# Kernel tuning notes

Hardware: AMD Instinct MI355X
Metric: run time of the kernel (lower is better)

Reference implementation:

```python
import jax, jax.numpy as jnp
import numpy as np

N_NODES = 100000
N_EDGES = 1200000
D_IN = 16
D_EDGE = 4
H = 64


def setup_inputs() -> dict:
    key = jax.random.key(0)
    ks = jax.random.split(key, 20)
    s = 0.05
    inp = {
        "src": jax.random.randint(ks[0], (N_EDGES,), 0, N_NODES),
        "dst": jax.random.randint(ks[1], (N_EDGES,), 0, N_NODES),
        "t": jax.random.uniform(ks[2], (N_EDGES,), dtype=jnp.float32),
        "x": jax.random.normal(ks[3], (N_NODES, D_IN), dtype=jnp.float32),
        "edge_attr": jax.random.normal(ks[4], (N_EDGES, D_EDGE), dtype=jnp.float32),
        # x_encoder
        "Wx": jax.random.normal(ks[5], (D_IN, H), dtype=jnp.float32) * s,
        "bx": jnp.zeros((H,), dtype=jnp.float32),
        # TransformerConv (heads=1, concat=False)
        "Wq": jax.random.normal(ks[6], (H, H), dtype=jnp.float32) * s,
        "bq": jnp.zeros((H,), dtype=jnp.float32),
        "Wk": jax.random.normal(ks[7], (H, H), dtype=jnp.float32) * s,
        "bk": jnp.zeros((H,), dtype=jnp.float32),
        "Wv": jax.random.normal(ks[8], (H, H), dtype=jnp.float32) * s,
        "bv": jnp.zeros((H,), dtype=jnp.float32),
        "We": jax.random.normal(ks[9], (D_EDGE, H), dtype=jnp.float32) * s,  # lin_edge, bias=False
        "Ws": jax.random.normal(ks[10], (H, H), dtype=jnp.float32) * s,  # lin_skip (root weight)
        "bs": jnp.zeros((H,), dtype=jnp.float32),
        # MLP head
        "W1": jax.random.normal(ks[11], (H, 8), dtype=jnp.float32) * s,
        "b1": jnp.zeros((8,), dtype=jnp.float32),
        "W2": jax.random.normal(ks[12], (8, 1), dtype=jnp.float32) * s,
        "b2": jnp.zeros((1,), dtype=jnp.float32),
    }
    return inp


def reference(src, dst, t, x, edge_attr, Wx, bx, Wq, bq, Wk, bk, Wv, bv, We, Ws, bs, W1, b1, W2, b2):
    # eval mode: dropouts are identity; TGN memory.update_state is a pure
    # side effect and does not influence the returned output.
    xe = x @ Wx + bx                             # [N, H]

    # TransformerConv, heads=1, concat=False, flow src -> dst
    q = xe @ Wq + bq                             # [N, H]
    k = xe @ Wk + bk                             # [N, H]
    v = xe @ Wv + bv                             # [N, H]
    e = edge_attr @ We                           # [E, H]

    k_e = k[src] + e                             # [E, H]
    v_e = v[src] + e                             # [E, H]
    alpha = jnp.sum(q[dst] * k_e, axis=-1) / jnp.sqrt(jnp.float32(H))  # [E]

    # softmax over incoming edges per destination node
    m = jax.ops.segment_max(alpha, dst, num_segments=N_NODES)
    a = jnp.exp(alpha - m[dst])
    denom = jax.ops.segment_sum(a, dst, num_segments=N_NODES)
    w = a / (denom[dst] + 1e-16)                 # [E]

    agg = jax.ops.segment_sum(v_e * w[:, None], dst, num_segments=N_NODES)  # [N, H]
    h_local = agg + (xe @ Ws + bs)               # root/skip connection

    h = h_local[dst]                             # [E, H]
    h = jax.nn.relu(h @ W1 + b1)                 # [E, 8]
    out = (h @ W2 + b2)[:, 0]                    # [E]
    return out
```

## Files before the change

### kernel.cpp

```cpp
#include <hip/hip_runtime.h>

#define H 64
#define CAP 48

#define OFF_M   0
#define OFF_U   256
#define OFF_W   272
#define OFF_C   288
#define OFF_R   292
#define OFF_R0  356
#define OFF_PV  360
#define OFF_PE  488
#define OFF_PS  520
#define OFF_BH1 648
#define OFF_BH2 656
#define CST_N   664

__device__ __forceinline__ unsigned f2bf(float f) {
    unsigned u = __float_as_uint(f);
    u += 0x7fffu + ((u >> 16) & 1u);
    return u >> 16;
}
__device__ __forceinline__ float bf_lo(unsigned u) { return __uint_as_float(u << 16); }
__device__ __forceinline__ float bf_hi(unsigned u) { return __uint_as_float(u & 0xffff0000u); }

__global__ __launch_bounds__(256) void k_fold(
    const float* __restrict__ Wx, const float* __restrict__ bx,
    const float* __restrict__ Wq, const float* __restrict__ bq,
    const float* __restrict__ Wk, const float* __restrict__ bk,
    const float* __restrict__ Wv, const float* __restrict__ bv,
    const float* __restrict__ Ws, const float* __restrict__ bs,
    const float* __restrict__ We, const float* __restrict__ W1,
    const float* __restrict__ b1, float* __restrict__ cst)
{
    __shared__ float sWf[4][16][64];
    __shared__ float sbf[4][64];
    const int t = threadIdx.x;
    const int c = t & 63, m = t >> 6;
    const float* W; const float* b;
    switch (m) {
        case 0:  W = Wq; b = bq; break;
        case 1:  W = Wk; b = bk; break;
        case 2:  W = Wv; b = bv; break;
        default: W = Ws; b = bs; break;
    }
    float acc[16];
#pragma unroll
    for (int i = 0; i < 16; ++i) acc[i] = 0.f;
    float bacc = b[c];
    for (int j = 0; j < 64; ++j) {
        const float wv = W[j * 64 + c];
        bacc += bx[j] * wv;
#pragma unroll
        for (int i = 0; i < 16; ++i) acc[i] += Wx[i * 64 + j] * wv;
    }
#pragma unroll
    for (int i = 0; i < 16; ++i) sWf[m][i][c] = acc[i];
    sbf[m][c] = bacc;
    __syncthreads();

    {
        const int i = t >> 4, j = t & 15;
        float s = 0.f;
        for (int cc = 0; cc < 64; ++cc) s += sWf[0][i][cc] * sWf[1][j][cc];
        cst[OFF_M + i * 16 + j] = s;
    }
    if (t < 16) {
        float su = 0.f, sw = 0.f;
        for (int cc = 0; cc < 64; ++cc) {
            su += sWf[1][t][cc] * sbf[0][cc];
            sw += sWf[0][t][cc] * sbf[1][cc];
        }
        cst[OFF_U + t] = su;
        cst[OFF_W + t] = sw;
    }
    if (t == 0) {
        float s = 0.f;
        for (int cc = 0; cc < 64; ++cc) s += sbf[0][cc] * sbf[1][cc];
        cst[OFF_C] = s;
    }
    if (t < 64) {
        const int j = t >> 4, i = t & 15;
        float s = 0.f;
        for (int cc = 0; cc < 64; ++cc) s += We[j * 64 + cc] * sWf[0][i][cc];
        cst[OFF_R + j * 16 + i] = s;
    }
    if (t < 4) {
        float s = 0.f;
        for (int cc = 0; cc < 64; ++cc) s += We[t * 64 + cc] * sbf[0][cc];
        cst[OFF_R0 + t] = s;
    }
    if (t < 128) {
        const int i = t >> 3, j = t & 7;
        float sv = 0.f, ss = 0.f;
        for (int cc = 0; cc < 64; ++cc) {
            const float w1 = W1[cc * 8 + j];
            sv += sWf[2][i][cc] * w1;
            ss += sWf[3][i][cc] * w1;
        }
        cst[OFF_PV + i * 8 + j] = sv;
        cst[OFF_PS + i * 8 + j] = ss;
    }
    if (t < 32) {
        const int mm = t >> 3, j = t & 7;
        float s = 0.f;
        for (int cc = 0; cc < 64; ++cc) s += We[mm * 64 + cc] * W1[cc * 8 + j];
        cst[OFF_PE + mm * 8 + j] = s;
    }
    if (t < 8) {
        float s1 = 0.f, s2 = 0.f;
        for (int cc = 0; cc < 64; ++cc) {
            const float w1 = W1[cc * 8 + t];
            s1 += sbf[2][cc] * w1;
            s2 += sbf[3][cc] * w1;
        }
        cst[OFF_BH1 + t] = s1;
        cst[OFF_BH2 + t] = s2 + b1[t];
    }
}

__global__ __launch_bounds__(256) void k_fill(
    const int* __restrict__ src, const int* __restrict__ dst,
    const float4* __restrict__ ea4,
    int* __restrict__ cursor, int4* __restrict__ csr, int E)
{
    const int e = blockIdx.x * 256 + threadIdx.x;
    if (e >= E) return;
    const int s = src[e];
    const int d = dst[e];
    const float4 A = ea4[e];
    const int pos = atomicAdd(&cursor[d], 1);
    if (pos < CAP) {
        int4 ent;
        ent.x = s;
        ent.y = e;
        ent.z = (int)(f2bf(A.x) | (f2bf(A.y) << 16));
        ent.w = (int)(f2bf(A.z) | (f2bf(A.w) << 16));
        csr[(size_t)d * CAP + pos] = ent;
    }
}

__global__ __launch_bounds__(256) void k_node_agg(
    const int* __restrict__ degp, const int4* __restrict__ csr,
    const float* __restrict__ x, const float* __restrict__ cst,
    const float* __restrict__ W2, const float* __restrict__ b2,
    float* __restrict__ out, int N)
{
    const int t = threadIdx.x;
    const int l = t & 63;
    const int w = t >> 6;
    const int n = blockIdx.x * 4 + w;
    if (n >= N) return;
    const int grp = l >> 4;
    const int cg  = l & 15;

    const int deg = min(degp[n], CAP);
    const size_t nbase = (size_t)n * CAP;

    const float xd = x[(size_t)n * 16 + cg];

    float y = cst[OFF_U + cg];
#pragma unroll
    for (int i = 0; i < 16; ++i)
        y += __shfl(xd, i) * cst[OFF_M + i * 16 + cg];

    float pr0 = cst[OFF_R + 0 * 16 + cg] * xd;
    float pr1 = cst[OFF_R + 1 * 16 + cg] * xd;
    float pr2 = cst[OFF_R + 2 * 16 + cg] * xd;
    float pr3 = cst[OFF_R + 3 * 16 + cg] * xd;
    float pcd = cst[OFF_W + cg] * xd;
#pragma unroll
    for (int d = 1; d < 16; d <<= 1) {
        pr0 += __shfl_xor(pr0, d);
        pr1 += __shfl_xor(pr1, d);
        pr2 += __shfl_xor(pr2, d);
        pr3 += __shfl_xor(pr3, d);
        pcd += __shfl_xor(pcd, d);
    }
    const float r0 = pr0 + cst[OFF_R0 + 0];
    const float r1 = pr1 + cst[OFF_R0 + 1];
    const float r2 = pr2 + cst[OFF_R0 + 2];
    const float r3 = pr3 + cst[OFF_R0 + 3];
    const float cd = pcd + cst[OFF_C];

    float T = 0.f, S0 = 0.f, S1 = 0.f, S2 = 0.f, S3 = 0.f, den = 0.f;

    for (int base = 0; base < deg; base += 8) {
        const int ia = base + grp;
        const int ib = base + 4 + grp;
        const bool va = ia < deg;
        const bool vb = ib < deg;
        const int4 Ea = csr[nbase + (va ? ia : 0)];
        const int4 Eb = csr[nbase + (vb ? ib : 0)];
        const float xsa = x[(size_t)Ea.x * 16 + cg];
        const float xsb = x[(size_t)Eb.x * 16 + cg];
        {
            const float A0 = bf_lo((unsigned)Ea.z), A1 = bf_hi((unsigned)Ea.z);
            const float A2 = bf_lo((unsigned)Ea.w), A3 = bf_hi((unsigned)Ea.w);
            float p = y * xsa;
            p += __shfl_xor(p, 1);
            p += __shfl_xor(p, 2);
            p += __shfl_xor(p, 4);
            p += __shfl_xor(p, 8);
            p += cd + A0 * r0 + A1 * r1 + A2 * r2 + A3 * r3;
            const float a = va ? __expf(p * 0.125f) : 0.f;
            T += a * xsa;
            S0 += a * A0; S1 += a * A1; S2 += a * A2; S3 += a * A3;
            den += a;
        }
        {
            const float A0 = bf_lo((unsigned)Eb.z), A1 = bf_hi((unsigned)Eb.z);
            const float A2 = bf_lo((unsigned)Eb.w), A3 = bf_hi((unsigned)Eb.w);
            float p = y * xsb;
            p += __shfl_xor(p, 1);
            p += __shfl_xor(p, 2);
            p += __shfl_xor(p, 4);
            p += __shfl_xor(p, 8);
            p += cd + A0 * r0 + A1 * r1 + A2 * r2 + A3 * r3;
            const float a = vb ? __expf(p * 0.125f) : 0.f;
            T += a * xsb;
            S0 += a * A0; S1 += a * A1; S2 += a * A2; S3 += a * A3;
            den += a;
        }
    }

    T   += __shfl_xor(T, 16);   T   += __shfl_xor(T, 32);
    den += __shfl_xor(den, 16); den += __shfl_xor(den, 32);
    S0  += __shfl_xor(S0, 16);  S0  += __shfl_xor(S0, 32);
    S1  += __shfl_xor(S1, 16);  S1  += __shfl_xor(S1, 32);
    S2  += __shfl_xor(S2, 16);  S2  += __shfl_xor(S2, 32);
    S3  += __shfl_xor(S3, 16);  S3  += __shfl_xor(S3, 32);

    const float inv = 1.f / (den + 1e-16f);
    const float Ti = T * inv;

    float hp[8];
#pragma unroll
    for (int j = 0; j < 8; ++j)
        hp[j] = Ti * cst[OFF_PV + cg * 8 + j] + xd * cst[OFF_PS + cg * 8 + j];
#pragma unroll
    for (int j = 0; j < 8; ++j) {
        hp[j] += __shfl_xor(hp[j], 1);
        hp[j] += __shfl_xor(hp[j], 2);
        hp[j] += __shfl_xor(hp[j], 4);
        hp[j] += __shfl_xor(hp[j], 8);
    }
    const float dinv = den * inv;
    float val = b2[0];
#pragma unroll
    for (int j = 0; j < 8; ++j) {
        const float hid = hp[j]
            + inv * (S0 * cst[OFF_PE + 0 * 8 + j] + S1 * cst[OFF_PE + 1 * 8 + j]
                   + S2 * cst[OFF_PE + 2 * 8 + j] + S3 * cst[OFF_PE + 3 * 8 + j])
            + dinv * cst[OFF_BH1 + j] + cst[OFF_BH2 + j];
        val += fmaxf(hid, 0.f) * W2[j];
    }

    for (int i = l; i < deg; i += 64)
        out[csr[nbase + i].y] = val;
}

extern "C" void kernel_launch(void* const* d_in, const int* in_sizes, int n_in,
                              void* d_out, int out_size, void* d_ws, size_t ws_size,
                              hipStream_t stream)
{
    const int*   src = (const int*)d_in[0];
    const int*   dst = (const int*)d_in[1];
    const float* x   = (const float*)d_in[3];
    const float* ea  = (const float*)d_in[4];
    const float* Wx  = (const float*)d_in[5];
    const float* bx  = (const float*)d_in[6];
    const float* Wq  = (const float*)d_in[7];
    const float* bq  = (const float*)d_in[8];
    const float* Wk  = (const float*)d_in[9];
    const float* bk  = (const float*)d_in[10];
    const float* Wv  = (const float*)d_in[11];
    const float* bv  = (const float*)d_in[12];
    const float* We  = (const float*)d_in[13];
    const float* Ws  = (const float*)d_in[14];
    const float* bs  = (const float*)d_in[15];
    const float* W1  = (const float*)d_in[16];
    const float* b1  = (const float*)d_in[17];
    const float* W2  = (const float*)d_in[18];
    const float* b2  = (const float*)d_in[19];

    const int E = in_sizes[0];
    const int N = in_sizes[3] / 16;
    float* out = (float*)d_out;

    int4* csr   = (int4*)d_ws;
    int* cursor = (int*)(csr + (size_t)N * CAP);
    float* cst  = (float*)(cursor + N);

    hipMemsetAsync(cursor, 0, (size_t)N * sizeof(int), stream);

    k_fold<<<1, 256, 0, stream>>>(Wx, bx, Wq, bq, Wk, bk, Wv, bv, Ws, bs,
                                  We, W1, b1, cst);

    k_fill<<<(E + 255) / 256, 256, 0, stream>>>(
        src, dst, (const float4*)ea, cursor, csr, E);

    k_node_agg<<<(N + 3) / 4, 256, 0, stream>>>(
        cursor, csr, x, cst, W2, b2, out, N);
}
```

Measured before the change: 299.5 us.

## Fuse weight fold into fill kernel, pad cursors, use nontemporal CSR stores

The single-block weight-folding kernel now runs as block 0 of the edge-fill kernel, which saves one launch. Per-node atomic cursors are padded to a 64-byte stride so that atomics on different destinations no longer share a cache line. CSR entries are written with nontemporal stores to reduce cache pollution. In exchange, the cursor memset grows sixteenfold and reading degrees in the aggregation kernel becomes strided and less coalesced.

Result: no change. 299.9 us (+0.1%).

```diff
diff --git a/kernel.cpp b/kernel.cpp
--- a/kernel.cpp
+++ b/kernel.cpp
@@ -2,6 +2,9 @@
 
 #define H 64
 #define CAP 48
+#define CSTRIDE 16
+
+typedef int nint4 __attribute__((ext_vector_type(4)));
 
 #define OFF_M   0
 #define OFF_U   256
@@ -24,7 +27,7 @@
 __device__ __forceinline__ float bf_lo(unsigned u) { return __uint_as_float(u << 16); }
 __device__ __forceinline__ float bf_hi(unsigned u) { return __uint_as_float(u & 0xffff0000u); }
 
-__global__ __launch_bounds__(256) void k_fold(
+__device__ void do_fold(
     const float* __restrict__ Wx, const float* __restrict__ bx,
     const float* __restrict__ Wq, const float* __restrict__ bq,
     const float* __restrict__ Wk, const float* __restrict__ bk,
@@ -122,26 +125,37 @@
 __global__ __launch_bounds__(256) void k_fill(
     const int* __restrict__ src, const int* __restrict__ dst,
     const float4* __restrict__ ea4,
-    int* __restrict__ cursor, int4* __restrict__ csr, int E)
+    int* __restrict__ cursor, nint4* __restrict__ csr, int E,
+    const float* __restrict__ Wx, const float* __restrict__ bx,
+    const float* __restrict__ Wq, const float* __restrict__ bq,
+    const float* __restrict__ Wk, const float* __restrict__ bk,
+    const float* __restrict__ Wv, const float* __restrict__ bv,
+    const float* __restrict__ Ws, const float* __restrict__ bs,
+    const float* __restrict__ We, const float* __restrict__ W1,
+    const float* __restrict__ b1, float* __restrict__ cst)
 {
-    const int e = blockIdx.x * 256 + threadIdx.x;
+    if (blockIdx.x == 0) {
+        do_fold(Wx, bx, Wq, bq, Wk, bk, Wv, bv, Ws, bs, We, W1, b1, cst);
+        return;
+    }
+    const int e = (blockIdx.x - 1) * 256 + threadIdx.x;
     if (e >= E) return;
     const int s = src[e];
     const int d = dst[e];
     const float4 A = ea4[e];
-    const int pos = atomicAdd(&cursor[d], 1);
+    const int pos = atomicAdd(&cursor[(size_t)d * CSTRIDE], 1);
     if (pos < CAP) {
-        int4 ent;
+        nint4 ent;
         ent.x = s;
         ent.y = e;
         ent.z = (int)(f2bf(A.x) | (f2bf(A.y) << 16));
         ent.w = (int)(f2bf(A.z) | (f2bf(A.w) << 16));
-        csr[(size_t)d * CAP + pos] = ent;
+        __builtin_nontemporal_store(ent, &csr[(size_t)d * CAP + pos]);
     }
 }
 
 __global__ __launch_bounds__(256) void k_node_agg(
-    const int* __restrict__ degp, const int4* __restrict__ csr,
+    const int* __restrict__ degp, const nint4* __restrict__ csr,
     const float* __restrict__ x, const float* __restrict__ cst,
     const float* __restrict__ W2, const float* __restrict__ b2,
     float* __restrict__ out, int N)
@@ -154,7 +168,7 @@
     const int grp = l >> 4;
     const int cg  = l & 15;
 
-    const int deg = min(degp[n], CAP);
+    const int deg = min(degp[(size_t)n * CSTRIDE], CAP);
     const size_t nbase = (size_t)n * CAP;
 
     const float xd = x[(size_t)n * 16 + cg];
@@ -190,8 +204,8 @@
         const int ib = base + 4 + grp;
         const bool va = ia < deg;
         const bool vb = ib < deg;
-        const int4 Ea = csr[nbase + (va ? ia : 0)];
-        const int4 Eb = csr[nbase + (vb ? ib : 0)];
+        const nint4 Ea = csr[nbase + (va ? ia : 0)];
+        const nint4 Eb = csr[nbase + (vb ? ib : 0)];
         const float xsa = x[(size_t)Ea.x * 16 + cg];
         const float xsb = x[(size_t)Eb.x * 16 + cg];
         {
@@ -288,17 +302,16 @@
     const int N = in_sizes[3] / 16;
     float* out = (float*)d_out;
 
-    int4* csr   = (int4*)d_ws;
+    nint4* csr  = (nint4*)d_ws;
     int* cursor = (int*)(csr + (size_t)N * CAP);
-    float* cst  = (float*)(cursor + N);
-
-    hipMemsetAsync(cursor, 0, (size_t)N * sizeof(int), stream);
-
-    k_fold<<<1, 256, 0, stream>>>(Wx, bx, Wq, bq, Wk, bk, Wv, bv, Ws, bs,
-                                  We, W1, b1, cst);
-
-    k_fill<<<(E + 255) / 256, 256, 0, stream>>>(
-        src, dst, (const float4*)ea, cursor, csr, E);
+    float* cst  = (float*)(cursor + (size_t)N * CSTRIDE);
+
+    hipMemsetAsync(cursor, 0, (size_t)N * CSTRIDE * sizeof(int), stream);
+
+    const int nbE = (E + 255) / 256;
+    k_fill<<<nbE + 1, 256, 0, stream>>>(
+        src, dst, (const float4*)ea, cursor, csr, E,
+        Wx, bx, Wq, bq, Wk, bk, Wv, bv, Ws, bs, We, W1, b1, cst);
 
     k_node_agg<<<(N + 3) / 4, 256, 0, stream>>>(
         cursor, csr, x, cst, W2, b2, out, N);
```
